# Kernel optimization log

Measured on AMD Instinct MI355X. Metric: run time of the kernel, lower is better.

The kernel has to match this reference:

```python
import jax, jax.numpy as jnp
import numpy as np

N_NODES = 50000
DEG = 32
HEADS = 4
OUT_F = 16
IN_F = 64
NEG_SLOPE = 0.01  # jax.nn.leaky_relu default


def setup_inputs() -> dict:
    key = jax.random.key(0)
    k_adj, k_mask, k_q, k_qw, k_kw, k_aw = jax.random.split(key, 6)
    adj = jax.random.randint(k_adj, (N_NODES, DEG), 0, N_NODES)
    pad = jax.random.uniform(k_mask, (N_NODES, DEG)) < 0.1
    adj = jnp.where(pad, -1, adj)
    Q = jax.random.normal(k_q, (IN_F, N_NODES), dtype=jnp.float32)
    qw_scale = 2 * np.sqrt(6.0 / (IN_F + OUT_F * HEADS))
    kw_scale = qw_scale
    a_scale = 2 * np.sqrt(6.0 / (OUT_F + HEADS))
    query_weight = (jax.random.uniform(k_qw, (HEADS, OUT_F, IN_F)) - 0.5) * qw_scale
    key_weight = (jax.random.uniform(k_kw, (HEADS, OUT_F, IN_F)) - 0.5) * kw_scale
    attn_weight = (jax.random.uniform(k_aw, (HEADS, OUT_F)) - 0.5) * a_scale
    return {
        'adj': adj,
        'Q': Q,
        'query_weight': query_weight.astype(jnp.float32),
        'key_weight': key_weight.astype(jnp.float32),
        'attn_weight': attn_weight.astype(jnp.float32),
    }


def reference(adj, Q, query_weight, key_weight, attn_weight):
    # K defaults to Q (self-attention over graph)
    K = Q
    # project keys: [H, O, N], then gather neighbors -> [H, O, N, deg]
    Ko = jnp.einsum('hoi,in->hon', key_weight, K)[..., adj]
    # project queries: [H, O, N]
    Qo = jnp.einsum('hoi,in->hon', query_weight, Q)
    # per-edge pre-activation and attention logits
    X = jax.nn.leaky_relu(Qo[..., None] + Ko, negative_slope=NEG_SLOPE)
    X = jnp.einsum('honk,ho->hnk', X, attn_weight)  # [H, N, deg]
    X = jnp.where(adj == -1, -jnp.inf, X)
    # rows with zero valid neighbors -> zero logits (uniform softmax, masked later)
    X = jnp.where((adj != -1).sum(-1, keepdims=True) == 0, 0.0, X)
    attn = jax.nn.softmax(X, axis=-1)
    # weighted aggregate of gathered keys -> [H, O, N]
    return jnp.einsum('hnk,honk->hon', jnp.where(adj == -1, 0.0, attn), Ko)
```

## Files before the change

kernel.cpp:

```cpp
#include <hip/hip_runtime.h>
#include <math.h>

#define DEG 32
#define NHO 64
#define NPW 4
#define NPB 16

typedef short  frag8  __attribute__((ext_vector_type(8)));
typedef float  f32x4  __attribute__((ext_vector_type(4)));

template <int CTRL>
__device__ __forceinline__ float dpp_add(float v) {
    int t = __builtin_amdgcn_update_dpp(0, __float_as_int(v), CTRL, 0xF, 0xF, true);
    return v + __int_as_float(t);
}

__device__ __forceinline__ unsigned bf16_rne(float f) {
    unsigned u = __float_as_uint(f);
    return (u + 0x7fffu + ((u >> 16) & 1u)) >> 16;
}

__global__ __launch_bounds__(256) void proj_mfma_kernel(
    const float* __restrict__ Q,
    const float* __restrict__ Wq,
    const float* __restrict__ Wk,
    unsigned short* __restrict__ Pqb,
    unsigned short* __restrict__ Pkb,
    int N)
{
    __shared__ unsigned qlds[64 * 33];
    __shared__ unsigned wlds[128 * 33];

    int t  = threadIdx.x;
    int n0 = blockIdx.x * 64;

    {
        int l    = t >> 1;
        int half = t & 1;
        const float* wr = (l < 64 ? Wq + (size_t)l * 64
                                  : Wk + (size_t)(l - 64) * 64) + half * 32;
#pragma unroll
        for (int r = 0; r < 16; r++) {
            float f0 = wr[2 * r], f1 = wr[2 * r + 1];
            wlds[l * 33 + half * 16 + r] = bf16_rne(f0) | (bf16_rne(f1) << 16);
        }
    }
    {
        int n  = t & 63;
        int gn = n0 + n;
        bool act = (gn < N);
#pragma unroll
        for (int r = 0; r < 8; r++) {
            int dp = (t >> 6) * 8 + r;
            int k  = dp * 2;
            float f0 = act ? Q[(size_t)k * N + gn] : 0.f;
            float f1 = act ? Q[(size_t)(k + 1) * N + gn] : 0.f;
            qlds[n * 33 + dp] = bf16_rne(f0) | (bf16_rne(f1) << 16);
        }
    }
    __syncthreads();

    int lane = t & 63;
    int w    = t >> 6;
    int li   = lane & 15;
    int quad = lane >> 4;

    f32x4 acc[8];
#pragma unroll
    for (int ot = 0; ot < 8; ot++) acc[ot] = (f32x4){0.f, 0.f, 0.f, 0.f};

#pragma unroll
    for (int ks = 0; ks < 2; ks++) {
        union { unsigned u[4]; frag8 f; } A;
        int abase = (w * 16 + li) * 33 + ks * 16 + quad * 4;
#pragma unroll
        for (int c = 0; c < 4; c++) A.u[c] = qlds[abase + c];
#pragma unroll
        for (int ot = 0; ot < 8; ot++) {
            union { unsigned u[4]; frag8 f; } B;
            int bbase = (ot * 16 + li) * 33 + ks * 16 + quad * 4;
#pragma unroll
            for (int c = 0; c < 4; c++) B.u[c] = wlds[bbase + c];
            acc[ot] = __builtin_amdgcn_mfma_f32_16x16x32_bf16(A.f, B.f, acc[ot],
                                                              0, 0, 0);
        }
    }

#pragma unroll
    for (int ot = 0; ot < 8; ot++) {
#pragma unroll
        for (int r = 0; r < 4; r++) {
            int node = n0 + w * 16 + quad * 4 + r;
            if (node < N) {
                unsigned short v = (unsigned short)bf16_rne(acc[ot][r]);
                if (ot < 4)
                    Pqb[(size_t)node * NHO + ot * 16 + li] = v;
                else
                    Pkb[(size_t)node * NHO + (ot - 4) * 16 + li] = v;
            }
        }
    }
}


__device__ __forceinline__ float swz_x16(float v) {
    return __int_as_float(__builtin_amdgcn_ds_swizzle(__float_as_int(v), 0x401F));
}
__device__ __forceinline__ float bprm(int addr, float v) {
    return __int_as_float(__builtin_amdgcn_ds_bpermute(addr, __float_as_int(v)));
}

__device__ __forceinline__ void gat_gather(uint2 (&dst)[8],
                                           const int4 lo, const int4 hi,
                                           const uint2* __restrict__ Pk64,
                                           int sl) {
    dst[0] = Pk64[(size_t)(lo.x < 0 ? 0 : lo.x) * 16 + sl];
    dst[1] = Pk64[(size_t)(lo.y < 0 ? 0 : lo.y) * 16 + sl];
    dst[2] = Pk64[(size_t)(lo.z < 0 ? 0 : lo.z) * 16 + sl];
    dst[3] = Pk64[(size_t)(lo.w < 0 ? 0 : lo.w) * 16 + sl];
    dst[4] = Pk64[(size_t)(hi.x < 0 ? 0 : hi.x) * 16 + sl];
    dst[5] = Pk64[(size_t)(hi.y < 0 ? 0 : hi.y) * 16 + sl];
    dst[6] = Pk64[(size_t)(hi.z < 0 ? 0 : hi.z) * 16 + sl];
    dst[7] = Pk64[(size_t)(hi.w < 0 ? 0 : hi.w) * 16 + sl];
}

__device__ __forceinline__ unsigned gat_vmask(const int4 lo, const int4 hi) {
    unsigned vm = 0;
    vm |= (lo.x >= 0) ? 1u   : 0u;
    vm |= (lo.y >= 0) ? 2u   : 0u;
    vm |= (lo.z >= 0) ? 4u   : 0u;
    vm |= (lo.w >= 0) ? 8u   : 0u;
    vm |= (hi.x >= 0) ? 16u  : 0u;
    vm |= (hi.y >= 0) ? 32u  : 0u;
    vm |= (hi.z >= 0) ? 64u  : 0u;
    vm |= (hi.w >= 0) ? 128u : 0u;
    return vm;
}

__device__ __forceinline__ void gat_compute(
    const uint2 (&kv)[8], unsigned vm, uint2 qraw,
    float c1_0, float c1_1, float c1_2, float c1_3,
    float c2_0, float c2_1, float c2_2, float c2_3,
    int slot, int sl, int bprm_x32, int col,
    float (&tile)[NHO][NPB + 1])
{
    float qp0 = __uint_as_float(qraw.x << 16);
    float qp1 = __uint_as_float(qraw.x & 0xffff0000u);
    float qp2 = __uint_as_float(qraw.y << 16);
    float qp3 = __uint_as_float(qraw.y & 0xffff0000u);

    float c1q = c1_0 * qp0;
    c1q = fmaf(c1_1, qp1, c1q);
    c1q = fmaf(c1_2, qp2, c1q);
    c1q = fmaf(c1_3, qp3, c1q);

    float s = 0.f, a0 = 0.f, a1 = 0.f, a2 = 0.f, a3 = 0.f;
#pragma unroll
    for (int t = 0; t < 8; t++) {
        float kv0 = __uint_as_float(kv[t].x << 16);
        float kv1 = __uint_as_float(kv[t].x & 0xffff0000u);
        float kv2 = __uint_as_float(kv[t].y << 16);
        float kv3 = __uint_as_float(kv[t].y & 0xffff0000u);
        float x0 = qp0 + kv0, x1 = qp1 + kv1;
        float x2 = qp2 + kv2, x3 = qp3 + kv3;
        float c = fmaf(c1_0, kv0, c1q);
        c = fmaf(c1_1, kv1, c);
        c = fmaf(c1_2, kv2, c);
        c = fmaf(c1_3, kv3, c);
        c = fmaf(c2_0, fabsf(x0), c);
        c = fmaf(c2_1, fabsf(x1), c);
        c = fmaf(c2_2, fabsf(x2), c);
        c = fmaf(c2_3, fabsf(x3), c);
        c = dpp_add<0xB1>(c);
        c = dpp_add<0x4E>(c);
        float p = __builtin_amdgcn_exp2f(c);
        p = (vm & (1u << t)) ? p : 0.f;
        s += p;
        a0 = fmaf(p, kv0, a0);
        a1 = fmaf(p, kv1, a1);
        a2 = fmaf(p, kv2, a2);
        a3 = fmaf(p, kv3, a3);
    }

    s  += swz_x16(s);
    a0 += swz_x16(a0);
    a1 += swz_x16(a1);
    a2 += swz_x16(a2);
    a3 += swz_x16(a3);
    s  += bprm(bprm_x32, s);
    a0 += bprm(bprm_x32, a0);
    a1 += bprm(bprm_x32, a1);
    a2 += bprm(bprm_x32, a2);
    a3 += bprm(bprm_x32, a3);

    float rs = (s > 0.f) ? __builtin_amdgcn_rcpf(s) : 0.f;
    if (slot == 0) {
        tile[4 * sl + 0][col] = a0 * rs;
        tile[4 * sl + 1][col] = a1 * rs;
        tile[4 * sl + 2][col] = a2 * rs;
        tile[4 * sl + 3][col] = a3 * rs;
    }
}

__global__ __launch_bounds__(256, 8) void gat_kernel(
    const int*            __restrict__ adj,
    const unsigned short* __restrict__ Pqb,
    const unsigned short* __restrict__ Pkb,
    const float*          __restrict__ aw,
    float*                __restrict__ out,
    int N)
{
    __shared__ float tile[NHO][NPB + 1];

    int l    = threadIdx.x & 63;
    int wv   = threadIdx.x >> 6;
    int sl   = l & 15;
    int slot = l >> 4;

    const uint2* Pk64 = (const uint2*)Pkb;
    const uint2* Pq64 = (const uint2*)Pqb;

    float4 awq = *(const float4*)(aw + 4 * sl);
    const float L2E = 1.44269504f;
    float c1_0 = 0.505f * L2E * awq.x, c2_0 = 0.495f * L2E * awq.x;
    float c1_1 = 0.505f * L2E * awq.y, c2_1 = 0.495f * L2E * awq.y;
    float c1_2 = 0.505f * L2E * awq.z, c2_2 = 0.495f * L2E * awq.z;
    float c1_3 = 0.505f * L2E * awq.w, c2_3 = 0.495f * L2E * awq.w;

    int bprm_x32 = (l ^ 32) * 4;
    int nbase = blockIdx.x * NPB + wv * NPW;

    if (nbase + NPW <= N) {
        const int* ap0 = adj + (size_t)nbase * DEG + slot * 8;
        int4  lo   = *(const int4*)ap0;
        int4  hi   = *(const int4*)(ap0 + 4);
        uint2 qraw = Pq64[(size_t)nbase * 16 + sl];

#pragma unroll
        for (int ni = 0; ni < NPW; ni++) {
            uint2 kv[8];
            gat_gather(kv, lo, hi, Pk64, sl);
            unsigned vm  = gat_vmask(lo, hi);
            uint2    cqr = qraw;
            if (ni + 1 < NPW) {
                const int* ap = adj + (size_t)(nbase + ni + 1) * DEG + slot * 8;
                lo   = *(const int4*)ap;
                hi   = *(const int4*)(ap + 4);
                qraw = Pq64[(size_t)(nbase + ni + 1) * 16 + sl];
            }
            gat_compute(kv, vm, cqr,
                        c1_0, c1_1, c1_2, c1_3, c2_0, c2_1, c2_2, c2_3,
                        slot, sl, bprm_x32, wv * NPW + ni, tile);
        }
    } else {
#pragma unroll 1
        for (int ni = 0; ni < NPW; ni++) {
            int n = nbase + ni;
            if (n < N) {
                const int* ap = adj + (size_t)n * DEG + slot * 8;
                int4 lo = *(const int4*)ap;
                int4 hi = *(const int4*)(ap + 4);
                uint2 qraw = Pq64[(size_t)n * 16 + sl];
                uint2 kv[8];
                gat_gather(kv, lo, hi, Pk64, sl);
                unsigned vm = gat_vmask(lo, hi);
                gat_compute(kv, vm, qraw,
                            c1_0, c1_1, c1_2, c1_3, c2_0, c2_1, c2_2, c2_3,
                            slot, sl, bprm_x32, wv * NPW + ni, tile);
            }
        }
    }
    __syncthreads();

    int n0 = blockIdx.x * NPB;
    int lr = threadIdx.x >> 2;
    int c4 = threadIdx.x & 3;
    int nc = n0 + c4 * 4;
    float4 v = make_float4(tile[lr][c4 * 4 + 0], tile[lr][c4 * 4 + 1],
                           tile[lr][c4 * 4 + 2], tile[lr][c4 * 4 + 3]);
    if (nc + 3 < N) {
        *(float4*)(out + (size_t)lr * N + nc) = v;
    } else {
#pragma unroll
        for (int e = 0; e < 4; e++)
            if (nc + e < N) out[(size_t)lr * N + nc + e] = (&v.x)[e];
    }
}

extern "C" void kernel_launch(void* const* d_in, const int* in_sizes, int n_in,
                              void* d_out, int out_size, void* d_ws, size_t ws_size,
                              hipStream_t stream) {
    const int*   adj = (const int*)  d_in[0];
    const float* Q   = (const float*)d_in[1];
    const float* qw  = (const float*)d_in[2];
    const float* kw  = (const float*)d_in[3];
    const float* aw  = (const float*)d_in[4];
    float*       out = (float*)d_out;

    int N = in_sizes[0] / DEG;

    unsigned short* Pqb = (unsigned short*)d_ws;
    unsigned short* Pkb = Pqb + (size_t)N * NHO;

    proj_mfma_kernel<<<(N + 63) / 64, 256, 0, stream>>>(Q, qw, kw, Pqb, Pkb, N);

    gat_kernel<<<(N + NPB - 1) / NPB, 256, 0, stream>>>(adj, Pqb, Pkb, aw, out, N);
}
```

Before: 109.2 us.

## Double-buffer neighbor gathers and double nodes per wave in GAT kernel

Doubles nodes per wave and per block (NPW 8, NPB 32) and lowers the launch-bounds occupancy hint from 8 to 4. It adds two register buffers for gathered key rows, so the gather for the next node is issued before computing the current one, while the adjacency for the node after that is prefetched. The aim is to hide gather latency behind compute in software instead of relying on many resident waves. The cost is more registers, lower occupancy and half as many blocks across the device.

```diff
diff --git a/kernel.cpp b/kernel.cpp
--- a/kernel.cpp
+++ b/kernel.cpp
@@ -3,8 +3,8 @@
 
 #define DEG 32
 #define NHO 64
-#define NPW 4
-#define NPB 16
+#define NPW 8
+#define NPB 32
 
 typedef short  frag8  __attribute__((ext_vector_type(8)));
 typedef float  f32x4  __attribute__((ext_vector_type(4)));
@@ -202,7 +202,7 @@
     }
 }
 
-__global__ __launch_bounds__(256, 8) void gat_kernel(
+__global__ __launch_bounds__(256, 4) void gat_kernel(
     const int*            __restrict__ adj,
     const unsigned short* __restrict__ Pqb,
     const unsigned short* __restrict__ Pkb,
@@ -231,28 +231,60 @@
     int nbase = blockIdx.x * NPB + wv * NPW;
 
     if (nbase + NPW <= N) {
+        uint2 kvA[8], kvB[8];
+
         const int* ap0 = adj + (size_t)nbase * DEG + slot * 8;
-        int4  lo   = *(const int4*)ap0;
-        int4  hi   = *(const int4*)(ap0 + 4);
-        uint2 qraw = Pq64[(size_t)nbase * 16 + sl];
+        int4 lo = *(const int4*)ap0;
+        int4 hi = *(const int4*)(ap0 + 4);
+        uint2 qrA = Pq64[(size_t)nbase * 16 + sl];
+        gat_gather(kvA, lo, hi, Pk64, sl);
+        unsigned vmA = gat_vmask(lo, hi);
+
+        const int* ap1 = adj + (size_t)(nbase + 1) * DEG + slot * 8;
+        lo = *(const int4*)ap1;
+        hi = *(const int4*)(ap1 + 4);
+        uint2 qrB = Pq64[(size_t)(nbase + 1) * 16 + sl];
+        unsigned vmB = 0;
 
 #pragma unroll
         for (int ni = 0; ni < NPW; ni++) {
-            uint2 kv[8];
-            gat_gather(kv, lo, hi, Pk64, sl);
-            unsigned vm  = gat_vmask(lo, hi);
-            uint2    cqr = qraw;
-            if (ni + 1 < NPW) {
-                const int* ap = adj + (size_t)(nbase + ni + 1) * DEG + slot * 8;
-                lo   = *(const int4*)ap;
-                hi   = *(const int4*)(ap + 4);
-                qraw = Pq64[(size_t)(nbase + ni + 1) * 16 + sl];
+            int col = wv * NPW + ni;
+            if ((ni & 1) == 0) {
+                uint2    qcur = qrA;
+                unsigned vmc  = vmA;
+                if (ni + 1 < NPW) {
+                    gat_gather(kvB, lo, hi, Pk64, sl);
+                    vmB = gat_vmask(lo, hi);
+                }
+                if (ni + 2 < NPW) {
+                    const int* ap = adj + (size_t)(nbase + ni + 2) * DEG + slot * 8;
+                    lo  = *(const int4*)ap;
+                    hi  = *(const int4*)(ap + 4);
+                    qrA = Pq64[(size_t)(nbase + ni + 2) * 16 + sl];
+                }
+                gat_compute(kvA, vmc, qcur,
+                            c1_0, c1_1, c1_2, c1_3, c2_0, c2_1, c2_2, c2_3,
+                            slot, sl, bprm_x32, col, tile);
+            } else {
+                uint2    qcur = qrB;
+                unsigned vmc  = vmB;
+                if (ni + 1 < NPW) {
+                    gat_gather(kvA, lo, hi, Pk64, sl);
+                    vmA = gat_vmask(lo, hi);
+                }
+                if (ni + 2 < NPW) {
+                    const int* ap = adj + (size_t)(nbase + ni + 2) * DEG + slot * 8;
+                    lo  = *(const int4*)ap;
+                    hi  = *(const int4*)(ap + 4);
+                    qrB = Pq64[(size_t)(nbase + ni + 2) * 16 + sl];
+                }
+                gat_compute(kvB, vmc, qcur,
+                            c1_0, c1_1, c1_2, c1_3, c2_0, c2_1, c2_2, c2_3,
+                            slot, sl, bprm_x32, col, tile);
             }
-            gat_compute(kv, vm, cqr,
-                        c1_0, c1_1, c1_2, c1_3, c2_0, c2_1, c2_2, c2_3,
-                        slot, sl, bprm_x32, wv * NPW + ni, tile);
         }
     } else {
+        uint2 kvA[8];
 #pragma unroll 1
         for (int ni = 0; ni < NPW; ni++) {
             int n = nbase + ni;
@@ -261,10 +293,9 @@
                 int4 lo = *(const int4*)ap;
                 int4 hi = *(const int4*)(ap + 4);
                 uint2 qraw = Pq64[(size_t)n * 16 + sl];
-                uint2 kv[8];
-                gat_gather(kv, lo, hi, Pk64, sl);
+                gat_gather(kvA, lo, hi, Pk64, sl);
                 unsigned vm = gat_vmask(lo, hi);
-                gat_compute(kv, vm, qraw,
+                gat_compute(kvA, vm, qraw,
                             c1_0, c1_1, c1_2, c1_3, c2_0, c2_1, c2_2, c2_3,
                             slot, sl, bprm_x32, wv * NPW + ni, tile);
             }
@@ -274,16 +305,20 @@
 
     int n0 = blockIdx.x * NPB;
     int lr = threadIdx.x >> 2;
-    int c4 = threadIdx.x & 3;
-    int nc = n0 + c4 * 4;
-    float4 v = make_float4(tile[lr][c4 * 4 + 0], tile[lr][c4 * 4 + 1],
-                           tile[lr][c4 * 4 + 2], tile[lr][c4 * 4 + 3]);
-    if (nc + 3 < N) {
-        *(float4*)(out + (size_t)lr * N + nc) = v;
-    } else {
-#pragma unroll
-        for (int e = 0; e < 4; e++)
-            if (nc + e < N) out[(size_t)lr * N + nc + e] = (&v.x)[e];
+    int c0 = (threadIdx.x & 3) * 8;
+#pragma unroll
+    for (int hlf = 0; hlf < 2; hlf++) {
+        int cc = c0 + hlf * 4;
+        int nc = n0 + cc;
+        float4 v = make_float4(tile[lr][cc + 0], tile[lr][cc + 1],
+                               tile[lr][cc + 2], tile[lr][cc + 3]);
+        if (nc + 3 < N) {
+            *(float4*)(out + (size_t)lr * N + nc) = v;
+        } else {
+#pragma unroll
+            for (int e = 0; e < 4; e++)
+                if (nc + e < N) out[(size_t)lr * N + nc + e] = (&v.x)[e];
+        }
     }
 }
 
```

New measurement: 109.7 us. No clear change (+0.5%).
